# Optimization experiments

Measured on AMD Instinct MI355X. Metric: run time of the kernel, lower is better.

Reference implementation:

```python
import jax, jax.numpy as jnp
import numpy as np

NUM_SKILLS = 1000
DIM_S = 64
SIZE_M = 64
B, T = 64, 200


def setup_inputs() -> dict:
    key = jax.random.key(0)
    ks = jax.random.split(key, 16)
    skills = jax.random.randint(ks[0], (B, T), 0, NUM_SKILLS)
    responses = jax.random.randint(ks[1], (B, T), 0, 2)
    s = 1.0 / np.sqrt(DIM_S)
    return {
        "skills": skills,
        "responses": responses,
        "k_emb": jax.random.normal(ks[2], (NUM_SKILLS, DIM_S)) * s,
        "v_emb": jax.random.normal(ks[3], (2 * NUM_SKILLS, DIM_S)) * s,
        "Mk": jax.random.normal(ks[4], (SIZE_M, DIM_S)) * np.sqrt(2.0 / DIM_S),
        "Mv0": jax.random.normal(ks[5], (SIZE_M, DIM_S)) * np.sqrt(2.0 / DIM_S),
        "fW": jax.random.normal(ks[6], (DIM_S, 2 * DIM_S)) * (1.0 / np.sqrt(2 * DIM_S)),
        "fb": jnp.zeros((DIM_S,)),
        "eW": jax.random.normal(ks[7], (DIM_S, DIM_S)) * s,
        "eb": jnp.zeros((DIM_S,)),
        "aW": jax.random.normal(ks[8], (DIM_S, DIM_S)) * s,
        "ab": jnp.zeros((DIM_S,)),
        "pW": jax.random.normal(ks[9], (1, DIM_S)) * s,
        "pb": jnp.zeros((1,)),
    }


def reference(skills, responses, k_emb, v_emb, Mk, Mv0, fW, fb, eW, eb, aW, ab, pW, pb):
    # dropout is identity in eval mode
    masked_r = responses * (responses > -1).astype(responses.dtype)
    x = skills + NUM_SKILLS * masked_r            # [B, T]
    k = k_emb[skills]                              # [B, T, D]
    v = v_emb[x]                                   # [B, T, D]
    w = jax.nn.softmax(jnp.einsum('btd,md->btm', k, Mk), axis=-1)  # [B, T, M]
    e = jax.nn.sigmoid(v @ eW.T + eb)              # [B, T, D]
    a = jnp.tanh(v @ aW.T + ab)                    # [B, T, D]

    Mv_init = jnp.broadcast_to(Mv0, (skills.shape[0],) + Mv0.shape)  # [B, M, D]

    def step(Mvt, inp):
        wt, et, at = inp                           # [B,M], [B,D], [B,D]
        read = jnp.einsum('bm,bmd->bd', wt, Mvt)   # read BEFORE update (Mv[:, :-1])
        Mvt = Mvt * (1.0 - wt[:, :, None] * et[:, None, :]) + wt[:, :, None] * at[:, None, :]
        return Mvt, read

    xs = (jnp.swapaxes(w, 0, 1), jnp.swapaxes(e, 0, 1), jnp.swapaxes(a, 0, 1))
    _, reads = jax.lax.scan(step, Mv_init, xs)     # reads: [T, B, D]
    reads = jnp.swapaxes(reads, 0, 1)              # [B, T, D]

    f = jnp.tanh(jnp.concatenate([reads, k], axis=-1) @ fW.T + fb)  # [B, T, D]
    p = jax.nn.sigmoid(f @ pW.T + pb)[..., 0]      # [B, T]
    return p[:, 1:]                                # pred, [B, T-1]
```

## Files before the change

kernel.cpp:

```cpp
#include <hip/hip_runtime.h>
#include <hip/hip_bf16.h>
#include <stdint.h>

#define NSK 1000
#define TT  200
#define BB  64
#define NROW (BB * TT)
#define NOUT (BB * (TT-1))
#define CH  20
#define RW  8

__device__ __forceinline__ float lane_bcast(float v, int l) {
  return __uint_as_float(__builtin_amdgcn_readlane(__float_as_uint(v), l));
}
__device__ __forceinline__ unsigned ulane_bcast(unsigned v, int l) {
  return __builtin_amdgcn_readlane(v, l);
}
__device__ __forceinline__ float frcp(float x) { return __builtin_amdgcn_rcpf(x); }
__device__ __forceinline__ float sigm(float x) { return frcp(1.f + __expf(-x)); }
__device__ __forceinline__ float tanh_fast(float x) {
  return fmaf(-2.f, frcp(1.f + __expf(2.f * x)), 1.f);
}

typedef _Float16 half2v __attribute__((ext_vector_type(2)));
union H2U { unsigned u; half2v h; };
__device__ __forceinline__ unsigned pack2h(float a, float b) {
  H2U x; x.h = (half2v){(_Float16)a, (_Float16)b}; return x.u;
}
__device__ __forceinline__ unsigned short f16bits(float x) {
  H2U u; u.h = (half2v){(_Float16)x, (_Float16)0.f}; return (unsigned short)(u.u & 0xffffu);
}
__device__ __forceinline__ float f16lo(unsigned bits) {
  H2U u; u.u = bits; return (float)u.h.x;
}
__device__ __forceinline__ float f16hi(unsigned bits) {
  H2U u; u.u = bits; return (float)u.h.y;
}
__device__ __forceinline__ float dot2h(unsigned sp, unsigned wp, float acc) {
#if __has_builtin(__builtin_amdgcn_fdot2)
  H2U s, w; s.u = sp; w.u = wp;
  return __builtin_amdgcn_fdot2(s.h, w.h, acc, false);
#else
  H2U s, w; s.u = sp; w.u = wp;
  return fmaf((float)s.h.y, (float)w.h.y, fmaf((float)s.h.x, (float)w.h.x, acc));
#endif
}
__device__ __forceinline__ unsigned pack_pairs(float v) {
  const int lane = threadIdx.x & 63;
  float a = __shfl(v, 2 * lane);
  float b = __shfl(v, 2 * lane + 1);
  return pack2h(a, b);
}

__global__ __launch_bounds__(256) void wea_kernel(
    const int* __restrict__ skills, const int* __restrict__ responses,
    const float* __restrict__ k_emb, const float* __restrict__ v_emb,
    const float* __restrict__ Mk, const float* __restrict__ eW,
    const float* __restrict__ eb, const float* __restrict__ aW,
    const float* __restrict__ ab,
    unsigned* __restrict__ ea_ws, unsigned short* __restrict__ w16_ws)
{
  __shared__ unsigned sw[3 * 64 * 40];
  const int tid = threadIdx.x;
  for (int ch = tid; ch < 1536; ch += 256) {
    const int mat = ch >> 9, rem = ch & 511;
    const int j = rem >> 3, cc = rem & 7;
    const float4* src = (mat == 0) ? (const float4*)Mk
                      : (mat == 1) ? (const float4*)eW : (const float4*)aW;
    const float4 f0 = src[j * 16 + cc * 2];
    const float4 f1 = src[j * 16 + cc * 2 + 1];
    uint4 pk;
    pk.x = pack2h(f0.x, f0.y); pk.y = pack2h(f0.z, f0.w);
    pk.z = pack2h(f1.x, f1.y); pk.w = pack2h(f1.z, f1.w);
    *(uint4*)&sw[mat * 2560 + j * 40 + ((cc + j) & 7) * 4] = pk;
  }
  __syncthreads();

  const int wave = tid >> 6, lane = tid & 63;
  const float ebl = eb[lane], abl = ab[lane];
  const int r0 = (blockIdx.x * 4 + wave) * 2;

  float kv[2], vv[2];
  #pragma unroll
  for (int i = 0; i < 2; ++i) {
    const int sk = skills[r0 + i];
    int rr = responses[r0 + i]; rr = (rr > -1) ? rr : 0;
    kv[i] = k_emb[(size_t)sk * 64 + lane];
    vv[i] = v_emb[(size_t)(sk + NSK * rr) * 64 + lane];
  }
  unsigned kp[2], vp[2];
  #pragma unroll
  for (int i = 0; i < 2; ++i) { kp[i] = pack_pairs(kv[i]); vp[i] = pack_pairs(vv[i]); }

  float accK[2] = {0.f, 0.f}, accE[2] = {0.f, 0.f}, accA[2] = {0.f, 0.f};
  #pragma unroll 1
  for (int h = 0; h < 2; ++h) {
    uint4 qm[4], qe[4], qa[4];
    #pragma unroll
    for (int c = 0; c < 4; ++c) {
      const int off = lane * 40 + (((h * 4 + c) + lane) & 7) * 4;
      qm[c] = *(const uint4*)&sw[off];
      qe[c] = *(const uint4*)&sw[2560 + off];
      qa[c] = *(const uint4*)&sw[5120 + off];
    }
    #pragma unroll
    for (int i = 0; i < 2; ++i) {
      #pragma unroll
      for (int c = 0; c < 4; ++c) {
        const unsigned um[4] = {qm[c].x, qm[c].y, qm[c].z, qm[c].w};
        const unsigned ue[4] = {qe[c].x, qe[c].y, qe[c].z, qe[c].w};
        const unsigned ua[4] = {qa[c].x, qa[c].y, qa[c].z, qa[c].w};
        #pragma unroll
        for (int m = 0; m < 4; ++m) {
          const int idx = (h * 4 + c) * 4 + m;
          const unsigned spk = ulane_bcast(kp[i], idx);
          const unsigned spv = ulane_bcast(vp[i], idx);
          accK[i] = dot2h(spk, um[m], accK[i]);
          accE[i] = dot2h(spv, ue[m], accE[i]);
          accA[i] = dot2h(spv, ua[m], accA[i]);
        }
      }
    }
  }
  #pragma unroll
  for (int i = 0; i < 2; ++i) {
    const int row = r0 + i;
    float mx = accK[i];
    #pragma unroll
    for (int off = 32; off; off >>= 1) mx = fmaxf(mx, __shfl_xor(mx, off));
    float ex = __expf(accK[i] - mx);
    float sm = ex;
    #pragma unroll
    for (int off = 32; off; off >>= 1) sm += __shfl_xor(sm, off);
    const float wv  = ex * frcp(sm);
    const float evv = sigm(accE[i] + ebl);
    const float avv = tanh_fast(accA[i] + abl);
    ea_ws[(size_t)row * 64 + lane]  = pack2h(evv, avv);
    w16_ws[(size_t)row * 64 + lane] = f16bits(wv);
  }
}

__device__ __forceinline__ void load_chunk(
    const unsigned* __restrict__ eap, const unsigned short* __restrict__ wp,
    int t0, int wl, int lane, unsigned* eab, unsigned* wvb)
{
  #pragma unroll
  for (int k = 0; k < CH; ++k) {
    eab[k] = eap[(t0 + k) * 64 + lane];
    wvb[k] = (unsigned)wp[(t0 + k) * 64 + wl];
  }
}

__device__ __forceinline__ void compute_chunk(
    float* Mv, const unsigned* eab, const unsigned* wvb,
    float* __restrict__ red, int wave, int lane)
{
  #pragma unroll
  for (int k = 0; k < CH; ++k) {
    const float ev = f16lo(eab[k]), av = f16hi(eab[k]);
    float rp = 0.f;
    #pragma unroll
    for (int i = 0; i < RW; ++i) {
      const float wm = f16lo(ulane_bcast(wvb[k], i));
      rp = fmaf(wm, Mv[i], rp);
      float tp = fmaf(-ev, Mv[i], av);
      Mv[i] = fmaf(wm, tp, Mv[i]);
    }
    red[k * 256 + wave * 64 + lane] = rp;
  }
}

__device__ __forceinline__ void reduce_store(
    const float* __restrict__ red, int ch, int base, int wave, int lane,
    unsigned short* __restrict__ ps)
{
  #pragma unroll
  for (int u = 0; u < 5; ++u) {
    const int k = wave * 5 + u;
    const float* rr = red + k * 256;
    const float v = (rr[lane] + rr[64 + lane]) + (rr[128 + lane] + rr[192 + lane]);
    ps[(size_t)(base + ch * CH + k) * 64 + lane] = f16bits(v);
  }
}

__global__ __launch_bounds__(256) void scan_kernel(
    const float* __restrict__ Mv0,
    const unsigned* __restrict__ ea_ws, const unsigned short* __restrict__ w16_ws,
    unsigned short* __restrict__ p0, unsigned short* __restrict__ p1)
{
  __shared__ float red[2][CH * 256];
  const int b    = blockIdx.x >> 1;
  const int s    = blockIdx.x & 1;
  const int wave = threadIdx.x >> 6;
  const int lane = threadIdx.x & 63;
  const int base = b * TT;
  const int m0   = s * 32 + wave * RW;
  const int wl   = m0 + (lane & (RW - 1));
  unsigned short* ps = s ? p1 : p0;

  float Mv[RW];
  #pragma unroll
  for (int i = 0; i < RW; ++i) Mv[i] = Mv0[(size_t)(m0 + i) * 64 + lane];

  const unsigned* eap = ea_ws + (size_t)base * 64;
  const unsigned short* wp = w16_ws + (size_t)base * 64;

  unsigned ea0[CH], wv0[CH], ea1[CH], wv1[CH];
  load_chunk(eap, wp, 0, wl, lane, ea0, wv0);
  for (int ch = 0; ch < TT / CH; ch += 2) {
    if ((ch + 1) * CH < TT)
      load_chunk(eap, wp, (ch + 1) * CH, wl, lane, ea1, wv1);
    compute_chunk(Mv, ea0, wv0, red[0], wave, lane);
    __syncthreads();
    reduce_store(red[0], ch, base, wave, lane, ps);
    if ((ch + 2) * CH < TT)
      load_chunk(eap, wp, (ch + 2) * CH, wl, lane, ea0, wv0);
    if ((ch + 1) * CH < TT) {
      compute_chunk(Mv, ea1, wv1, red[1], wave, lane);
      __syncthreads();
      reduce_store(red[1], ch + 1, base, wave, lane, ps);
    }
  }
}

__global__ __launch_bounds__(256) void fp_kernel(
    const int* __restrict__ skills, const float* __restrict__ k_emb,
    const float* __restrict__ fW, const float* __restrict__ fb,
    const float* __restrict__ pW, const float* __restrict__ pb,
    const unsigned short* __restrict__ p0, const unsigned short* __restrict__ p1,
    float* __restrict__ out)
{
  __shared__ unsigned sf[64 * 72];
  const int tid = threadIdx.x;
  for (int ch = tid; ch < 1024; ch += 256) {
    const int j = ch >> 4, cc = ch & 15;
    const float4 f0 = ((const float4*)fW)[j * 32 + cc * 2];
    const float4 f1 = ((const float4*)fW)[j * 32 + cc * 2 + 1];
    uint4 pk;
    pk.x = pack2h(f0.x, f0.y); pk.y = pack2h(f0.z, f0.w);
    pk.z = pack2h(f1.x, f1.y); pk.w = pack2h(f1.z, f1.w);
    *(uint4*)&sf[j * 72 + ((cc + j) & 15) * 4] = pk;
  }
  __syncthreads();

  const int wave = tid >> 6, lane = tid & 63;
  const float fbl = fb[lane], pwl = pW[lane], pb0 = pb[0];
  const int p = blockIdx.x * 4 + wave;

  float rv[2], kc[2];
  int bsave[2], tsave[2];
  #pragma unroll
  for (int i = 0; i < 2; ++i) {
    const unsigned idx = 2u * p + i;
    const unsigned b = idx / 199u;
    const int row = (int)(idx + b + 1u);
    bsave[i] = (int)b; tsave[i] = (int)(idx - b * 199u);
    rv[i] = f16lo((unsigned)p0[(size_t)row * 64 + lane])
          + f16lo((unsigned)p1[(size_t)row * 64 + lane]);
    kc[i] = k_emb[(size_t)skills[row] * 64 + lane];
  }
  unsigned rvp[2], kvp[2];
  #pragma unroll
  for (int i = 0; i < 2; ++i) {
    rvp[i] = pack_pairs(rv[i]);
    kvp[i] = pack_pairs(kc[i]);
  }

  float acc[2] = {fbl, fbl};
  #pragma unroll 1
  for (int h = 0; h < 4; ++h) {
    uint4 qf[4];
    #pragma unroll
    for (int c = 0; c < 4; ++c)
      qf[c] = *(const uint4*)&sf[lane * 72 + (((h * 4 + c) + lane) & 15) * 4];
    #pragma unroll
    for (int i = 0; i < 2; ++i) {
      #pragma unroll
      for (int c = 0; c < 4; ++c) {
        const unsigned uu[4] = {qf[c].x, qf[c].y, qf[c].z, qf[c].w};
        #pragma unroll
        for (int m = 0; m < 4; ++m) {
          const int idx = (h * 4 + c) * 4 + m;
          const unsigned sp = (idx < 32) ? ulane_bcast(rvp[i], idx)
                                         : ulane_bcast(kvp[i], idx - 32);
          acc[i] = dot2h(sp, uu[m], acc[i]);
        }
      }
    }
  }

  float f0 = tanh_fast(acc[0]) * pwl;
  float f1 = tanh_fast(acc[1]) * pwl;
  #pragma unroll
  for (int off = 32; off; off >>= 1) {
    f0 += __shfl_xor(f0, off);
    f1 += __shfl_xor(f1, off);
  }
  if (lane == 0) {
    out[(size_t)bsave[0] * (TT - 1) + tsave[0]] = sigm(f0 + pb0);
    out[(size_t)bsave[1] * (TT - 1) + tsave[1]] = sigm(f1 + pb0);
  }
}

extern "C" void kernel_launch(void* const* d_in, const int* in_sizes, int n_in,
                              void* d_out, int out_size, void* d_ws, size_t ws_size,
                              hipStream_t stream) {
  const int* skills    = (const int*)d_in[0];
  const int* responses = (const int*)d_in[1];
  const float* k_emb   = (const float*)d_in[2];
  const float* v_emb   = (const float*)d_in[3];
  const float* Mk      = (const float*)d_in[4];
  const float* Mv0     = (const float*)d_in[5];
  const float* fW      = (const float*)d_in[6];
  const float* fb      = (const float*)d_in[7];
  const float* eW      = (const float*)d_in[8];
  const float* eb      = (const float*)d_in[9];
  const float* aW      = (const float*)d_in[10];
  const float* ab      = (const float*)d_in[11];
  const float* pW      = (const float*)d_in[12];
  const float* pb      = (const float*)d_in[13];

  unsigned* ea_ws       = (unsigned*)d_ws;
  unsigned short* w16_ws = (unsigned short*)(ea_ws + (size_t)NROW * 64);
  unsigned short* p0    = w16_ws + (size_t)NROW * 64;
  unsigned short* p1    = p0 + (size_t)NROW * 64;

  wea_kernel<<<dim3(NROW / 8), 256, 0, stream>>>(
      skills, responses, k_emb, v_emb, Mk, eW, eb, aW, ab, ea_ws, w16_ws);
  scan_kernel<<<dim3(BB * 2), 256, 0, stream>>>(Mv0, ea_ws, w16_ws, p0, p1);
  fp_kernel<<<dim3(NOUT / 8), 256, 0, stream>>>(
      skills, k_emb, fW, fb, pW, pb, p0, p1, (float*)d_out);
}
```

Baseline: 130.1 us.

## Fuse projection, scan and prediction into one per-sequence kernel with LDS staging

Replaces the three kernels (w/e/a projection, memory scan, prediction) with one kernel launched once per batch sequence at 512 threads. Intermediate w, e/a and read vectors are kept in LDS rather than global workspace, and each of the 8 waves scans 8 memory slots instead of splitting each sequence across two blocks. This removes two launches and the global round trips, but runs only 64 blocks, so the projection and prediction phases lose parallelism and the whole pipeline serializes within each block. Chunk size is halved and each scan chunk now needs two barriers.

```diff
diff --git a/kernel.cpp b/kernel.cpp
--- a/kernel.cpp
+++ b/kernel.cpp
@@ -1,18 +1,12 @@
 #include <hip/hip_runtime.h>
-#include <hip/hip_bf16.h>
 #include <stdint.h>
 
 #define NSK 1000
 #define TT  200
 #define BB  64
-#define NROW (BB * TT)
-#define NOUT (BB * (TT-1))
-#define CH  20
+#define CH  10
 #define RW  8
 
-__device__ __forceinline__ float lane_bcast(float v, int l) {
-  return __uint_as_float(__builtin_amdgcn_readlane(__float_as_uint(v), l));
-}
 __device__ __forceinline__ unsigned ulane_bcast(unsigned v, int l) {
   return __builtin_amdgcn_readlane(v, l);
 }
@@ -52,102 +46,14 @@
   return pack2h(a, b);
 }
 
-__global__ __launch_bounds__(256) void wea_kernel(
-    const int* __restrict__ skills, const int* __restrict__ responses,
-    const float* __restrict__ k_emb, const float* __restrict__ v_emb,
-    const float* __restrict__ Mk, const float* __restrict__ eW,
-    const float* __restrict__ eb, const float* __restrict__ aW,
-    const float* __restrict__ ab,
-    unsigned* __restrict__ ea_ws, unsigned short* __restrict__ w16_ws)
-{
-  __shared__ unsigned sw[3 * 64 * 40];
-  const int tid = threadIdx.x;
-  for (int ch = tid; ch < 1536; ch += 256) {
-    const int mat = ch >> 9, rem = ch & 511;
-    const int j = rem >> 3, cc = rem & 7;
-    const float4* src = (mat == 0) ? (const float4*)Mk
-                      : (mat == 1) ? (const float4*)eW : (const float4*)aW;
-    const float4 f0 = src[j * 16 + cc * 2];
-    const float4 f1 = src[j * 16 + cc * 2 + 1];
-    uint4 pk;
-    pk.x = pack2h(f0.x, f0.y); pk.y = pack2h(f0.z, f0.w);
-    pk.z = pack2h(f1.x, f1.y); pk.w = pack2h(f1.z, f1.w);
-    *(uint4*)&sw[mat * 2560 + j * 40 + ((cc + j) & 7) * 4] = pk;
-  }
-  __syncthreads();
-
-  const int wave = tid >> 6, lane = tid & 63;
-  const float ebl = eb[lane], abl = ab[lane];
-  const int r0 = (blockIdx.x * 4 + wave) * 2;
-
-  float kv[2], vv[2];
-  #pragma unroll
-  for (int i = 0; i < 2; ++i) {
-    const int sk = skills[r0 + i];
-    int rr = responses[r0 + i]; rr = (rr > -1) ? rr : 0;
-    kv[i] = k_emb[(size_t)sk * 64 + lane];
-    vv[i] = v_emb[(size_t)(sk + NSK * rr) * 64 + lane];
-  }
-  unsigned kp[2], vp[2];
-  #pragma unroll
-  for (int i = 0; i < 2; ++i) { kp[i] = pack_pairs(kv[i]); vp[i] = pack_pairs(vv[i]); }
-
-  float accK[2] = {0.f, 0.f}, accE[2] = {0.f, 0.f}, accA[2] = {0.f, 0.f};
-  #pragma unroll 1
-  for (int h = 0; h < 2; ++h) {
-    uint4 qm[4], qe[4], qa[4];
-    #pragma unroll
-    for (int c = 0; c < 4; ++c) {
-      const int off = lane * 40 + (((h * 4 + c) + lane) & 7) * 4;
-      qm[c] = *(const uint4*)&sw[off];
-      qe[c] = *(const uint4*)&sw[2560 + off];
-      qa[c] = *(const uint4*)&sw[5120 + off];
-    }
-    #pragma unroll
-    for (int i = 0; i < 2; ++i) {
-      #pragma unroll
-      for (int c = 0; c < 4; ++c) {
-        const unsigned um[4] = {qm[c].x, qm[c].y, qm[c].z, qm[c].w};
-        const unsigned ue[4] = {qe[c].x, qe[c].y, qe[c].z, qe[c].w};
-        const unsigned ua[4] = {qa[c].x, qa[c].y, qa[c].z, qa[c].w};
-        #pragma unroll
-        for (int m = 0; m < 4; ++m) {
-          const int idx = (h * 4 + c) * 4 + m;
-          const unsigned spk = ulane_bcast(kp[i], idx);
-          const unsigned spv = ulane_bcast(vp[i], idx);
-          accK[i] = dot2h(spk, um[m], accK[i]);
-          accE[i] = dot2h(spv, ue[m], accE[i]);
-          accA[i] = dot2h(spv, ua[m], accA[i]);
-        }
-      }
-    }
-  }
-  #pragma unroll
-  for (int i = 0; i < 2; ++i) {
-    const int row = r0 + i;
-    float mx = accK[i];
-    #pragma unroll
-    for (int off = 32; off; off >>= 1) mx = fmaxf(mx, __shfl_xor(mx, off));
-    float ex = __expf(accK[i] - mx);
-    float sm = ex;
-    #pragma unroll
-    for (int off = 32; off; off >>= 1) sm += __shfl_xor(sm, off);
-    const float wv  = ex * frcp(sm);
-    const float evv = sigm(accE[i] + ebl);
-    const float avv = tanh_fast(accA[i] + abl);
-    ea_ws[(size_t)row * 64 + lane]  = pack2h(evv, avv);
-    w16_ws[(size_t)row * 64 + lane] = f16bits(wv);
-  }
-}
-
-__device__ __forceinline__ void load_chunk(
-    const unsigned* __restrict__ eap, const unsigned short* __restrict__ wp,
+__device__ __forceinline__ void load_chunk_l(
+    const unsigned* __restrict__ sea, const unsigned short* __restrict__ swr,
     int t0, int wl, int lane, unsigned* eab, unsigned* wvb)
 {
   #pragma unroll
   for (int k = 0; k < CH; ++k) {
-    eab[k] = eap[(t0 + k) * 64 + lane];
-    wvb[k] = (unsigned)wp[(t0 + k) * 64 + wl];
+    eab[k] = sea[(t0 + k) * 64 + lane];
+    wvb[k] = (unsigned)swr[(t0 + k) * 64 + wl];
   }
 }
 
@@ -166,73 +72,54 @@
       float tp = fmaf(-ev, Mv[i], av);
       Mv[i] = fmaf(wm, tp, Mv[i]);
     }
-    red[k * 256 + wave * 64 + lane] = rp;
-  }
-}
-
-__device__ __forceinline__ void reduce_store(
-    const float* __restrict__ red, int ch, int base, int wave, int lane,
-    unsigned short* __restrict__ ps)
+    red[k * 512 + wave * 64 + lane] = rp;
+  }
+}
+
+__device__ __forceinline__ void reduce_store_l(
+    const float* __restrict__ red, int t0, int wave, int lane,
+    unsigned short* __restrict__ swr)
 {
-  #pragma unroll
-  for (int u = 0; u < 5; ++u) {
-    const int k = wave * 5 + u;
-    const float* rr = red + k * 256;
-    const float v = (rr[lane] + rr[64 + lane]) + (rr[128 + lane] + rr[192 + lane]);
-    ps[(size_t)(base + ch * CH + k) * 64 + lane] = f16bits(v);
-  }
-}
-
-__global__ __launch_bounds__(256) void scan_kernel(
-    const float* __restrict__ Mv0,
-    const unsigned* __restrict__ ea_ws, const unsigned short* __restrict__ w16_ws,
-    unsigned short* __restrict__ p0, unsigned short* __restrict__ p1)
-{
-  __shared__ float red[2][CH * 256];
-  const int b    = blockIdx.x >> 1;
-  const int s    = blockIdx.x & 1;
-  const int wave = threadIdx.x >> 6;
-  const int lane = threadIdx.x & 63;
-  const int base = b * TT;
-  const int m0   = s * 32 + wave * RW;
-  const int wl   = m0 + (lane & (RW - 1));
-  unsigned short* ps = s ? p1 : p0;
-
-  float Mv[RW];
-  #pragma unroll
-  for (int i = 0; i < RW; ++i) Mv[i] = Mv0[(size_t)(m0 + i) * 64 + lane];
-
-  const unsigned* eap = ea_ws + (size_t)base * 64;
-  const unsigned short* wp = w16_ws + (size_t)base * 64;
-
-  unsigned ea0[CH], wv0[CH], ea1[CH], wv1[CH];
-  load_chunk(eap, wp, 0, wl, lane, ea0, wv0);
-  for (int ch = 0; ch < TT / CH; ch += 2) {
-    if ((ch + 1) * CH < TT)
-      load_chunk(eap, wp, (ch + 1) * CH, wl, lane, ea1, wv1);
-    compute_chunk(Mv, ea0, wv0, red[0], wave, lane);
-    __syncthreads();
-    reduce_store(red[0], ch, base, wave, lane, ps);
-    if ((ch + 2) * CH < TT)
-      load_chunk(eap, wp, (ch + 2) * CH, wl, lane, ea0, wv0);
-    if ((ch + 1) * CH < TT) {
-      compute_chunk(Mv, ea1, wv1, red[1], wave, lane);
-      __syncthreads();
-      reduce_store(red[1], ch + 1, base, wave, lane, ps);
-    }
-  }
-}
-
-__global__ __launch_bounds__(256) void fp_kernel(
-    const int* __restrict__ skills, const float* __restrict__ k_emb,
+  for (int k = wave; k < CH; k += 8) {
+    const float* rr = red + k * 512;
+    const float v = ((rr[lane] + rr[64 + lane]) + (rr[128 + lane] + rr[192 + lane]))
+                  + ((rr[256 + lane] + rr[320 + lane]) + (rr[384 + lane] + rr[448 + lane]));
+    swr[(t0 + k) * 64 + lane] = f16bits(v);
+  }
+}
+
+__global__ __launch_bounds__(512, 1) void dkvmn_fused(
+    const int* __restrict__ skills, const int* __restrict__ responses,
+    const float* __restrict__ k_emb, const float* __restrict__ v_emb,
+    const float* __restrict__ Mk, const float* __restrict__ Mv0,
     const float* __restrict__ fW, const float* __restrict__ fb,
+    const float* __restrict__ eW, const float* __restrict__ eb,
+    const float* __restrict__ aW, const float* __restrict__ ab,
     const float* __restrict__ pW, const float* __restrict__ pb,
-    const unsigned short* __restrict__ p0, const unsigned short* __restrict__ p1,
     float* __restrict__ out)
 {
-  __shared__ unsigned sf[64 * 72];
-  const int tid = threadIdx.x;
-  for (int ch = tid; ch < 1024; ch += 256) {
+  __shared__ unsigned sw[7680];
+  __shared__ unsigned sf[4608];
+  __shared__ unsigned sea[TT * 64];
+  __shared__ unsigned short swr[TT * 64];
+
+  const int tid  = threadIdx.x;
+  const int wave = tid >> 6, lane = tid & 63;
+  const int b    = blockIdx.x;
+
+  for (int ch = tid; ch < 1536; ch += 512) {
+    const int mat = ch >> 9, rem = ch & 511;
+    const int j = rem >> 3, cc = rem & 7;
+    const float4* src = (mat == 0) ? (const float4*)Mk
+                      : (mat == 1) ? (const float4*)eW : (const float4*)aW;
+    const float4 f0 = src[j * 16 + cc * 2];
+    const float4 f1 = src[j * 16 + cc * 2 + 1];
+    uint4 pk;
+    pk.x = pack2h(f0.x, f0.y); pk.y = pack2h(f0.z, f0.w);
+    pk.z = pack2h(f1.x, f1.y); pk.w = pack2h(f1.z, f1.w);
+    *(uint4*)&sw[mat * 2560 + j * 40 + ((cc + j) & 7) * 4] = pk;
+  }
+  for (int ch = tid; ch < 1024; ch += 512) {
     const int j = ch >> 4, cc = ch & 15;
     const float4 f0 = ((const float4*)fW)[j * 32 + cc * 2];
     const float4 f1 = ((const float4*)fW)[j * 32 + cc * 2 + 1];
@@ -243,62 +130,157 @@
   }
   __syncthreads();
 
-  const int wave = tid >> 6, lane = tid & 63;
-  const float fbl = fb[lane], pwl = pW[lane], pb0 = pb[0];
-  const int p = blockIdx.x * 4 + wave;
-
-  float rv[2], kc[2];
-  int bsave[2], tsave[2];
-  #pragma unroll
-  for (int i = 0; i < 2; ++i) {
-    const unsigned idx = 2u * p + i;
-    const unsigned b = idx / 199u;
-    const int row = (int)(idx + b + 1u);
-    bsave[i] = (int)b; tsave[i] = (int)(idx - b * 199u);
-    rv[i] = f16lo((unsigned)p0[(size_t)row * 64 + lane])
-          + f16lo((unsigned)p1[(size_t)row * 64 + lane]);
-    kc[i] = k_emb[(size_t)skills[row] * 64 + lane];
-  }
-  unsigned rvp[2], kvp[2];
-  #pragma unroll
-  for (int i = 0; i < 2; ++i) {
-    rvp[i] = pack_pairs(rv[i]);
-    kvp[i] = pack_pairs(kc[i]);
-  }
-
-  float acc[2] = {fbl, fbl};
-  #pragma unroll 1
-  for (int h = 0; h < 4; ++h) {
-    uint4 qf[4];
+  {
+    const float ebl = eb[lane], abl = ab[lane];
+    for (int it = 0; it < 13; ++it) {
+      const int rr0 = it * 16 + wave * 2;
+      if (rr0 > 198) continue;
+
+      float kv[2], vv[2];
+      #pragma unroll
+      for (int i = 0; i < 2; ++i) {
+        const int row = b * TT + rr0 + i;
+        const int sk = skills[row];
+        int rr = responses[row]; rr = (rr > -1) ? rr : 0;
+        kv[i] = k_emb[(size_t)sk * 64 + lane];
+        vv[i] = v_emb[(size_t)(sk + NSK * rr) * 64 + lane];
+      }
+      unsigned kp[2], vp[2];
+      #pragma unroll
+      for (int i = 0; i < 2; ++i) { kp[i] = pack_pairs(kv[i]); vp[i] = pack_pairs(vv[i]); }
+
+      float accK[2] = {0.f, 0.f}, accE[2] = {0.f, 0.f}, accA[2] = {0.f, 0.f};
+      #pragma unroll 1
+      for (int h = 0; h < 2; ++h) {
+        uint4 qm[4], qe[4], qa[4];
+        #pragma unroll
+        for (int c = 0; c < 4; ++c) {
+          const int off = lane * 40 + (((h * 4 + c) + lane) & 7) * 4;
+          qm[c] = *(const uint4*)&sw[off];
+          qe[c] = *(const uint4*)&sw[2560 + off];
+          qa[c] = *(const uint4*)&sw[5120 + off];
+        }
+        #pragma unroll
+        for (int i = 0; i < 2; ++i) {
+          #pragma unroll
+          for (int c = 0; c < 4; ++c) {
+            const unsigned um[4] = {qm[c].x, qm[c].y, qm[c].z, qm[c].w};
+            const unsigned ue[4] = {qe[c].x, qe[c].y, qe[c].z, qe[c].w};
+            const unsigned ua[4] = {qa[c].x, qa[c].y, qa[c].z, qa[c].w};
+            #pragma unroll
+            for (int m = 0; m < 4; ++m) {
+              const int idx = (h * 4 + c) * 4 + m;
+              const unsigned spk = ulane_bcast(kp[i], idx);
+              const unsigned spv = ulane_bcast(vp[i], idx);
+              accK[i] = dot2h(spk, um[m], accK[i]);
+              accE[i] = dot2h(spv, ue[m], accE[i]);
+              accA[i] = dot2h(spv, ua[m], accA[i]);
+            }
+          }
+        }
+      }
+      #pragma unroll
+      for (int i = 0; i < 2; ++i) {
+        const int r = rr0 + i;
+        float mx = accK[i];
+        #pragma unroll
+        for (int off = 32; off; off >>= 1) mx = fmaxf(mx, __shfl_xor(mx, off));
+        float ex = __expf(accK[i] - mx);
+        float sm = ex;
+        #pragma unroll
+        for (int off = 32; off; off >>= 1) sm += __shfl_xor(sm, off);
+        const float wv  = ex * frcp(sm);
+        const float evv = sigm(accE[i] + ebl);
+        const float avv = tanh_fast(accA[i] + abl);
+        sea[r * 64 + lane] = pack2h(evv, avv);
+        swr[r * 64 + lane] = f16bits(wv);
+      }
+    }
+  }
+  __syncthreads();
+
+  {
+    float* red = (float*)sw;
+    const int m0 = wave * RW;
+    const int wl = m0 + (lane & (RW - 1));
+    float Mv[RW];
     #pragma unroll
-    for (int c = 0; c < 4; ++c)
-      qf[c] = *(const uint4*)&sf[lane * 72 + (((h * 4 + c) + lane) & 15) * 4];
-    #pragma unroll
-    for (int i = 0; i < 2; ++i) {
-      #pragma unroll
-      for (int c = 0; c < 4; ++c) {
-        const unsigned uu[4] = {qf[c].x, qf[c].y, qf[c].z, qf[c].w};
-        #pragma unroll
-        for (int m = 0; m < 4; ++m) {
-          const int idx = (h * 4 + c) * 4 + m;
-          const unsigned sp = (idx < 32) ? ulane_bcast(rvp[i], idx)
-                                         : ulane_bcast(kvp[i], idx - 32);
-          acc[i] = dot2h(sp, uu[m], acc[i]);
+    for (int i = 0; i < RW; ++i) Mv[i] = Mv0[(size_t)(m0 + i) * 64 + lane];
+
+    unsigned ea0[CH], wv0[CH], ea1[CH], wv1[CH];
+    load_chunk_l(sea, swr, 0, wl, lane, ea0, wv0);
+    for (int ch = 0; ch < TT / CH; ch += 2) {
+      load_chunk_l(sea, swr, (ch + 1) * CH, wl, lane, ea1, wv1);
+      compute_chunk(Mv, ea0, wv0, red, wave, lane);
+      __syncthreads();
+      reduce_store_l(red, ch * CH, wave, lane, swr);
+      __syncthreads();
+      if (ch + 2 < TT / CH)
+        load_chunk_l(sea, swr, (ch + 2) * CH, wl, lane, ea0, wv0);
+      compute_chunk(Mv, ea1, wv1, red, wave, lane);
+      __syncthreads();
+      reduce_store_l(red, (ch + 1) * CH, wave, lane, swr);
+      __syncthreads();
+    }
+  }
+
+  {
+    const float fbl = fb[lane], pwl = pW[lane], pb0 = pb[0];
+    for (int it = 0; it < 13; ++it) {
+      const int o0 = it * 16 + wave * 2;
+      if (o0 > 198) continue;
+      const int oB = (o0 + 1 <= 198) ? (o0 + 1) : o0;
+      const int oo[2] = {o0, oB};
+
+      float rv[2], kc[2];
+      #pragma unroll
+      for (int i = 0; i < 2; ++i) {
+        const int r = oo[i] + 1;
+        rv[i] = f16lo((unsigned)swr[r * 64 + lane]);
+        kc[i] = k_emb[(size_t)skills[b * TT + r] * 64 + lane];
+      }
+      unsigned rvp[2], kvp[2];
+      #pragma unroll
+      for (int i = 0; i < 2; ++i) {
+        rvp[i] = pack_pairs(rv[i]);
+        kvp[i] = pack_pairs(kc[i]);
+      }
+
+      float acc[2] = {fbl, fbl};
+      #pragma unroll 1
+      for (int h = 0; h < 4; ++h) {
+        uint4 qf[4];
+        #pragma unroll
+        for (int c = 0; c < 4; ++c)
+          qf[c] = *(const uint4*)&sf[lane * 72 + (((h * 4 + c) + lane) & 15) * 4];
+        #pragma unroll
+        for (int i = 0; i < 2; ++i) {
+          #pragma unroll
+          for (int c = 0; c < 4; ++c) {
+            const unsigned uu[4] = {qf[c].x, qf[c].y, qf[c].z, qf[c].w};
+            #pragma unroll
+            for (int m = 0; m < 4; ++m) {
+              const int idx = (h * 4 + c) * 4 + m;
+              const unsigned sp = (idx < 32) ? ulane_bcast(rvp[i], idx)
+                                             : ulane_bcast(kvp[i], idx - 32);
+              acc[i] = dot2h(sp, uu[m], acc[i]);
+            }
+          }
         }
       }
+
+      float f0 = tanh_fast(acc[0]) * pwl;
+      float f1 = tanh_fast(acc[1]) * pwl;
+      #pragma unroll
+      for (int off = 32; off; off >>= 1) {
+        f0 += __shfl_xor(f0, off);
+        f1 += __shfl_xor(f1, off);
+      }
+      if (lane == 0) {
+        out[(size_t)b * (TT - 1) + o0] = sigm(f0 + pb0);
+        if (oB != o0) out[(size_t)b * (TT - 1) + oB] = sigm(f1 + pb0);
+      }
     }
-  }
-
-  float f0 = tanh_fast(acc[0]) * pwl;
-  float f1 = tanh_fast(acc[1]) * pwl;
-  #pragma unroll
-  for (int off = 32; off; off >>= 1) {
-    f0 += __shfl_xor(f0, off);
-    f1 += __shfl_xor(f1, off);
-  }
-  if (lane == 0) {
-    out[(size_t)bsave[0] * (TT - 1) + tsave[0]] = sigm(f0 + pb0);
-    out[(size_t)bsave[1] * (TT - 1) + tsave[1]] = sigm(f1 + pb0);
   }
 }
 
@@ -319,15 +301,9 @@
   const float* ab      = (const float*)d_in[11];
   const float* pW      = (const float*)d_in[12];
   const float* pb      = (const float*)d_in[13];
-
-  unsigned* ea_ws       = (unsigned*)d_ws;
-  unsigned short* w16_ws = (unsigned short*)(ea_ws + (size_t)NROW * 64);
-  unsigned short* p0    = w16_ws + (size_t)NROW * 64;
-  unsigned short* p1    = p0 + (size_t)NROW * 64;
-
-  wea_kernel<<<dim3(NROW / 8), 256, 0, stream>>>(
-      skills, responses, k_emb, v_emb, Mk, eW, eb, aW, ab, ea_ws, w16_ws);
-  scan_kernel<<<dim3(BB * 2), 256, 0, stream>>>(Mv0, ea_ws, w16_ws, p0, p1);
-  fp_kernel<<<dim3(NOUT / 8), 256, 0, stream>>>(
-      skills, k_emb, fW, fb, pW, pb, p0, p1, (float*)d_out);
-}
+  (void)d_ws; (void)ws_size; (void)in_sizes; (void)n_in; (void)out_size;
+
+  dkvmn_fused<<<dim3(BB), 512, 0, stream>>>(
+      skills, responses, k_emb, v_emb, Mk, Mv0, fW, fb, eW, eb, aW, ab, pW, pb,
+      (float*)d_out);
+}
```

New measurement: 218.6 us. 1.68x slower.
